# Kernel optimization log

Measured on AMD Instinct MI355X. Metric: run time of the kernel, lower is better.

## Reference

```python
import jax, jax.numpy as jnp
import numpy as np

B = 4_194_304

def setup_inputs() -> dict:
    key = jax.random.key(0)
    k1, k2, k3, k4, k5 = jax.random.split(key, 5)
    return {
        "pred": jax.random.normal(k1, (B, 2), dtype=jnp.float32),
        "target": jax.random.normal(k2, (B, 1), dtype=jnp.float32),
        "prev_pci": jax.random.normal(k3, (B, 1), dtype=jnp.float32),
        "delta_time": jax.random.randint(k4, (B,), 0, 10, dtype=jnp.int32),
        "pv_values": jax.random.randint(k5, (B,), 0, 2, dtype=jnp.int32),
    }

def reference(pred, target, prev_pci, delta_time, pv_values):
    # pred: [B,2] -> lower/upper interval bounds, kept as [B,1] columns
    lower = pred[:, 0:1]
    upper = pred[:, 1:2]
    center = (lower + upper) * 0.5                    # [B,1]

    center_loss = jnp.mean((target - center) ** 2)
    width_loss = jnp.mean(upper - lower)
    valid_penalty = jnp.mean(jnp.maximum(lower - upper, 0.0))

    # Vectorized form of the per-sample conditional penalty:
    #   pv==0 & dt!=0 -> relu(center - prev)
    #   pv!=0 & dt!=0 -> relu(prev - center)
    #   dt==0         -> 0
    dt_nz = (delta_time != 0)[:, None]                # [B,1]
    pv_zero = (pv_values == 0)[:, None]               # [B,1]
    pen_up = jax.nn.relu(center - prev_pci)
    pen_dn = jax.nn.relu(prev_pci - center)
    per_sample = jnp.where(dt_nz & pv_zero, pen_up,
                  jnp.where(dt_nz & ~pv_zero, pen_dn, 0.0))
    direction_penalty = jnp.sum(per_sample)

    n = pv_values.shape[0]
    total = (center_loss * 1.5 + 0.1 * width_loss
             + 10.0 * valid_penalty + 0.5 * direction_penalty / n)
    return total
```

## Files before the change

kernel.cpp:

```cpp
#include <hip/hip_runtime.h>

#define THREADS 256
#define WAVE 64
#define GROUPS_PER_BLOCK (THREADS * 2)

__global__ __launch_bounds__(THREADS) void loss_reduce(
    const float4* __restrict__ pred4,
    const float4* __restrict__ tgt4,
    const float4* __restrict__ prev4,
    const int4*   __restrict__ dt4,
    const int4*   __restrict__ pv4,
    float* __restrict__ partials,
    int n4)
{
    int i0 = blockIdx.x * GROUPS_PER_BLOCK + threadIdx.x;
    int i1 = i0 + THREADS;
    bool v0 = (i0 < n4);
    bool v1 = (i1 < n4);

    float4 a0, a1, t0, q0;  int4 d0, e0;
    float4 b0, b1, t1, q1;  int4 d1, e1;

    if (v0) {
        a0 = pred4[2 * i0];
        a1 = pred4[2 * i0 + 1];
        t0 = tgt4[i0];
        q0 = prev4[i0];
        d0 = dt4[i0];
        e0 = pv4[i0];
    }
    if (v1) {
        b0 = pred4[2 * i1];
        b1 = pred4[2 * i1 + 1];
        t1 = tgt4[i1];
        q1 = prev4[i1];
        d1 = dt4[i1];
        e1 = pv4[i1];
    }

    float s0 = 0.f, s1 = 0.f, s2 = 0.f, s3 = 0.f;

    if (v0) {
        float lo[4]  = {a0.x, a0.z, a1.x, a1.z};
        float up[4]  = {a0.y, a0.w, a1.y, a1.w};
        float tga[4] = {t0.x, t0.y, t0.z, t0.w};
        float ppa[4] = {q0.x, q0.y, q0.z, q0.w};
        int   dta[4] = {d0.x, d0.y, d0.z, d0.w};
        int   pva[4] = {e0.x, e0.y, e0.z, e0.w};
#pragma unroll
        for (int j = 0; j < 4; ++j) {
            float c = 0.5f * (lo[j] + up[j]);
            float d = tga[j] - c;
            s0 += d * d;
            s1 += up[j] - lo[j];
            s2 += fmaxf(lo[j] - up[j], 0.0f);
            float diff = c - ppa[j];
            float pen = (pva[j] == 0) ? fmaxf(diff, 0.0f) : fmaxf(-diff, 0.0f);
            s3 += (dta[j] != 0) ? pen : 0.0f;
        }
    }
    if (v1) {
        float lo[4]  = {b0.x, b0.z, b1.x, b1.z};
        float up[4]  = {b0.y, b0.w, b1.y, b1.w};
        float tga[4] = {t1.x, t1.y, t1.z, t1.w};
        float ppa[4] = {q1.x, q1.y, q1.z, q1.w};
        int   dta[4] = {d1.x, d1.y, d1.z, d1.w};
        int   pva[4] = {e1.x, e1.y, e1.z, e1.w};
#pragma unroll
        for (int j = 0; j < 4; ++j) {
            float c = 0.5f * (lo[j] + up[j]);
            float d = tga[j] - c;
            s0 += d * d;
            s1 += up[j] - lo[j];
            s2 += fmaxf(lo[j] - up[j], 0.0f);
            float diff = c - ppa[j];
            float pen = (pva[j] == 0) ? fmaxf(diff, 0.0f) : fmaxf(-diff, 0.0f);
            s3 += (dta[j] != 0) ? pen : 0.0f;
        }
    }

    float w = 1.5f * s0 + 0.1f * s1 + 10.0f * s2 + 0.5f * s3;

#pragma unroll
    for (int off = 32; off > 0; off >>= 1)
        w += __shfl_down(w, off, WAVE);

    __shared__ float smem[THREADS / WAVE];
    if ((threadIdx.x & 63) == 0) smem[threadIdx.x >> 6] = w;
    __syncthreads();
    if (threadIdx.x == 0) {
        float acc = smem[0];
#pragma unroll
        for (int wv = 1; wv < THREADS / WAVE; ++wv) acc += smem[wv];
        partials[blockIdx.x] = acc;
    }
}

__global__ __launch_bounds__(THREADS) void loss_final(
    const float* __restrict__ partials, int nblocks,
    const float* __restrict__ pred, const float* __restrict__ tgt,
    const float* __restrict__ prev, const int* __restrict__ dt,
    const int* __restrict__ pvv,
    int tail_start, int n,
    float* __restrict__ out)
{
    float s = 0.f;
    for (int t = threadIdx.x; t < nblocks; t += THREADS)
        s += partials[t];

    if (threadIdx.x == 0) {
        for (int i = tail_start; i < n; ++i) {
            float lo = pred[2 * i], up = pred[2 * i + 1];
            float c = 0.5f * (lo + up);
            float d = tgt[i] - c;
            float pen = (pvv[i] == 0) ? fmaxf(c - prev[i], 0.f)
                                      : fmaxf(prev[i] - c, 0.f);
            s += 1.5f * d * d + 0.1f * (up - lo) + 10.0f * fmaxf(lo - up, 0.f)
               + 0.5f * ((dt[i] != 0) ? pen : 0.f);
        }
    }

#pragma unroll
    for (int off = 32; off > 0; off >>= 1)
        s += __shfl_down(s, off, WAVE);

    __shared__ float smem[THREADS / WAVE];
    if ((threadIdx.x & 63) == 0) smem[threadIdx.x >> 6] = s;
    __syncthreads();
    if (threadIdx.x == 0) {
        float acc = smem[0];
#pragma unroll
        for (int wv = 1; wv < THREADS / WAVE; ++wv) acc += smem[wv];
        out[0] = acc / (float)n;
    }
}

extern "C" void kernel_launch(void* const* d_in, const int* in_sizes, int n_in,
                              void* d_out, int out_size, void* d_ws, size_t ws_size,
                              hipStream_t stream) {
    const float* pred   = (const float*)d_in[0];
    const float* target = (const float*)d_in[1];
    const float* prev   = (const float*)d_in[2];
    const int*   dt     = (const int*)d_in[3];
    const int*   pv     = (const int*)d_in[4];
    float* out = (float*)d_out;

    int n  = in_sizes[3];
    int n4 = n >> 2;
    int nblocks = (n4 + GROUPS_PER_BLOCK - 1) / GROUPS_PER_BLOCK;

    float* partials = (float*)d_ws;

    loss_reduce<<<nblocks, THREADS, 0, stream>>>(
        (const float4*)pred, (const float4*)target, (const float4*)prev,
        (const int4*)dt, (const int4*)pv, partials, n4);

    loss_final<<<1, THREADS, 0, stream>>>(
        partials, nblocks, pred, target, prev, dt, pv, n4 * 4, n, out);
}
```

Before: 121.4 us.

## Fuse final reduction into main kernel via last-block atomic ticket

Merges the two-kernel reduction into one kernel. Each block writes its partial, fences, and takes an atomic ticket; the block that draws the last ticket sums all partials and the scalar tail. This removes the second kernel launch and its dependency gap, but adds a memset of the ticket before the launch plus an atomic and fence per block.

```diff
diff --git a/kernel.cpp b/kernel.cpp
--- a/kernel.cpp
+++ b/kernel.cpp
@@ -4,14 +4,19 @@
 #define WAVE 64
 #define GROUPS_PER_BLOCK (THREADS * 2)
 
-__global__ __launch_bounds__(THREADS) void loss_reduce(
+__global__ __launch_bounds__(THREADS) void loss_fused(
     const float4* __restrict__ pred4,
     const float4* __restrict__ tgt4,
     const float4* __restrict__ prev4,
     const int4*   __restrict__ dt4,
     const int4*   __restrict__ pv4,
     float* __restrict__ partials,
-    int n4)
+    unsigned int* __restrict__ ticket,
+    const float* __restrict__ pred, const float* __restrict__ tgt,
+    const float* __restrict__ prev, const int* __restrict__ dt,
+    const int* __restrict__ pvv,
+    int tail_start, int n, int nblocks, int n4,
+    float* __restrict__ out)
 {
     int i0 = blockIdx.x * GROUPS_PER_BLOCK + threadIdx.x;
     int i1 = i0 + THREADS;
@@ -86,6 +91,7 @@
         w += __shfl_down(w, off, WAVE);
 
     __shared__ float smem[THREADS / WAVE];
+    __shared__ bool is_last;
     if ((threadIdx.x & 63) == 0) smem[threadIdx.x >> 6] = w;
     __syncthreads();
     if (threadIdx.x == 0) {
@@ -93,17 +99,15 @@
 #pragma unroll
         for (int wv = 1; wv < THREADS / WAVE; ++wv) acc += smem[wv];
         partials[blockIdx.x] = acc;
+        __threadfence();
+        unsigned int old = atomicAdd(ticket, 1u);
+        is_last = (old == (unsigned int)(nblocks - 1));
     }
-}
+    __syncthreads();
+    if (!is_last) return;
 
-__global__ __launch_bounds__(THREADS) void loss_final(
-    const float* __restrict__ partials, int nblocks,
-    const float* __restrict__ pred, const float* __restrict__ tgt,
-    const float* __restrict__ prev, const int* __restrict__ dt,
-    const int* __restrict__ pvv,
-    int tail_start, int n,
-    float* __restrict__ out)
-{
+    __threadfence();
+
     float s = 0.f;
     for (int t = threadIdx.x; t < nblocks; t += THREADS)
         s += partials[t];
@@ -124,7 +128,7 @@
     for (int off = 32; off > 0; off >>= 1)
         s += __shfl_down(s, off, WAVE);
 
-    __shared__ float smem[THREADS / WAVE];
+    __syncthreads();
     if ((threadIdx.x & 63) == 0) smem[threadIdx.x >> 6] = s;
     __syncthreads();
     if (threadIdx.x == 0) {
@@ -149,12 +153,13 @@
     int n4 = n >> 2;
     int nblocks = (n4 + GROUPS_PER_BLOCK - 1) / GROUPS_PER_BLOCK;
 
-    float* partials = (float*)d_ws;
+    unsigned int* ticket = (unsigned int*)d_ws;
+    float* partials = (float*)((char*)d_ws + 256);
 
-    loss_reduce<<<nblocks, THREADS, 0, stream>>>(
+    hipMemsetAsync(d_ws, 0, sizeof(unsigned int), stream);
+
+    loss_fused<<<nblocks, THREADS, 0, stream>>>(
         (const float4*)pred, (const float4*)target, (const float4*)prev,
-        (const int4*)dt, (const int4*)pv, partials, n4);
-
-    loss_final<<<1, THREADS, 0, stream>>>(
-        partials, nblocks, pred, target, prev, dt, pv, n4 * 4, n, out);
+        (const int4*)dt, (const int4*)pv, partials, ticket,
+        pred, target, prev, dt, pv, n4 * 4, n, nblocks, n4, out);
 }
```

Result: slower. 214.9 us (+77.0%).
